# Performance work log

Measured on AMD Instinct MI355X. Metric: run time of the kernel, lower is better.

Reference implementation:

```python
import jax, jax.numpy as jnp
import numpy as np

D = 2048
H = 16
DH = D // H  # 128
B = 512
EPS = 1e-5


def _layernorm(x, g, b):
    m = jnp.mean(x, axis=-1, keepdims=True)
    v = jnp.mean((x - m) ** 2, axis=-1, keepdims=True)
    return (x - m) * jax.lax.rsqrt(v + EPS) * g + b


def setup_inputs() -> dict:
    key = jax.random.key(0)
    ks = jax.random.split(key, 16)
    s_in = 1.0 / np.sqrt(D)
    s_ff = 1.0 / np.sqrt(4 * D)
    return {
        "x": jax.random.normal(ks[0], (B, D), jnp.float32),
        # per-head q/k/v projections, stacked over heads: [H, D, DH]
        "Wq": jax.random.uniform(ks[1], (H, D, DH), jnp.float32, -s_in, s_in),
        "bq": jax.random.uniform(ks[2], (H, DH), jnp.float32, -s_in, s_in),
        "Wk": jax.random.uniform(ks[3], (H, D, DH), jnp.float32, -s_in, s_in),
        "bk": jax.random.uniform(ks[4], (H, DH), jnp.float32, -s_in, s_in),
        "Wv": jax.random.uniform(ks[5], (H, D, DH), jnp.float32, -s_in, s_in),
        "bv": jax.random.uniform(ks[6], (H, DH), jnp.float32, -s_in, s_in),
        "Wo": jax.random.uniform(ks[7], (D, D), jnp.float32, -s_in, s_in),
        "bo": jax.random.uniform(ks[8], (D,), jnp.float32, -s_in, s_in),
        "W1": jax.random.uniform(ks[9], (D, 4 * D), jnp.float32, -s_in, s_in),
        "b1": jax.random.uniform(ks[10], (4 * D,), jnp.float32, -s_in, s_in),
        "W2": jax.random.uniform(ks[11], (4 * D, D), jnp.float32, -s_ff, s_ff),
        "b2": jax.random.uniform(ks[12], (D,), jnp.float32, -s_ff, s_ff),
        "g1": jnp.ones((D,), jnp.float32),
        "be1": jnp.zeros((D,), jnp.float32),
        "g2": jnp.ones((D,), jnp.float32),
        "be2": jnp.zeros((D,), jnp.float32),
    }


def reference(x, Wq, bq, Wk, bk, Wv, bv, Wo, bo, W1, b1, W2, b2, g1, be1, g2, be2):
    # --- pre-norm attention branch ---
    h = _layernorm(x, g1, be1)                       # [B, D]
    q = jnp.einsum('bd,hde->bhe', h, Wq) + bq        # [B, H, DH]
    k = jnp.einsum('bd,hde->bhe', h, Wk) + bk
    v = jnp.einsum('bd,hde->bhe', h, Wv) + bv
    # outer-product 'attention' per sample: [B, H, DH, DH]
    attn = q[..., :, None] * k[..., None, :] / jnp.sqrt(jnp.float32(DH))
    attn = jax.nn.softmax(attn, axis=-1)
    o = jnp.einsum('bhij,bhj->bhi', attn, v)         # [B, H, DH]
    o = o.reshape(x.shape[0], H * DH)                # concat over heads
    x = x + o @ Wo + bo
    # --- pre-norm FFN branch ---
    h2 = _layernorm(x, g2, be2)
    x = x + jax.nn.relu(h2 @ W1 + b1) @ W2 + b2
    return x
```

## Files before the change

kernel.cpp:

```cpp
#include <hip/hip_runtime.h>
#include <hip/hip_bf16.h>
#include <math.h>


#define DDIM 2048
#define HHEADS 16
#define DHEAD 128
#define BROWS 512
#define LN_EPS 1e-5f

typedef __bf16 bf16x8_t __attribute__((ext_vector_type(8)));
typedef float f32x4_t __attribute__((ext_vector_type(4)));

#define GLD16(gptr, lptr)                                                     \
    __builtin_amdgcn_global_load_lds(                                         \
        (const __attribute__((address_space(1))) void*)(gptr),                \
        (__attribute__((address_space(3))) void*)(lptr), 16, 0, 0)

__global__ __launch_bounds__(256) void ln_kernel(const float* __restrict__ x,
                                                 const float* __restrict__ g,
                                                 const float* __restrict__ b,
                                                 __bf16* __restrict__ out) {
    const int row = blockIdx.x;
    const int tid = threadIdx.x;
    const float4* x4 = (const float4*)(x + (size_t)row * DDIM);
    float4 a = x4[2 * tid];
    float4 c = x4[2 * tid + 1];
    float s  = a.x + a.y + a.z + a.w + c.x + c.y + c.z + c.w;
    float s2 = a.x*a.x + a.y*a.y + a.z*a.z + a.w*a.w
             + c.x*c.x + c.y*c.y + c.z*c.z + c.w*c.w;
    #pragma unroll
    for (int off = 32; off > 0; off >>= 1) {
        s  += __shfl_down(s, off);
        s2 += __shfl_down(s2, off);
    }
    __shared__ float ps[4], ps2[4];
    __shared__ float mean_s, rstd_s;
    const int lane = tid & 63, w = tid >> 6;
    if (lane == 0) { ps[w] = s; ps2[w] = s2; }
    __syncthreads();
    if (tid == 0) {
        float S  = ps[0] + ps[1] + ps[2] + ps[3];
        float S2 = ps2[0] + ps2[1] + ps2[2] + ps2[3];
        float m  = S * (1.0f / DDIM);
        float var = S2 * (1.0f / DDIM) - m * m;
        mean_s = m;
        rstd_s = rsqrtf(var + LN_EPS);
    }
    __syncthreads();
    const float m = mean_s, r = rstd_s;
    const float4* g4 = (const float4*)g;
    const float4* b4 = (const float4*)b;
    float4 ga = g4[2 * tid], gb = g4[2 * tid + 1];
    float4 ba = b4[2 * tid], bb = b4[2 * tid + 1];
    bf16x8_t o;
    o[0] = (__bf16)((a.x - m) * r * ga.x + ba.x);
    o[1] = (__bf16)((a.y - m) * r * ga.y + ba.y);
    o[2] = (__bf16)((a.z - m) * r * ga.z + ba.z);
    o[3] = (__bf16)((a.w - m) * r * ga.w + ba.w);
    o[4] = (__bf16)((c.x - m) * r * gb.x + bb.x);
    o[5] = (__bf16)((c.y - m) * r * gb.y + bb.y);
    o[6] = (__bf16)((c.z - m) * r * gb.z + bb.z);
    o[7] = (__bf16)((c.w - m) * r * gb.w + bb.w);
    *(bf16x8_t*)(out + (size_t)row * DDIM + tid * 8) = o;
}

__global__ __launch_bounds__(256) void transpose_kernel(
    const float* __restrict__ src, __bf16* __restrict__ dst, int R, int C) {
    __shared__ float tile[32][33];
    const size_t bofs = (size_t)blockIdx.z * R * C;
    src += bofs;
    dst += bofs;
    const int c0 = blockIdx.x * 32, r0 = blockIdx.y * 32;
    const int tx = threadIdx.x & 31, ty = threadIdx.x >> 5;
    #pragma unroll
    for (int i = 0; i < 32; i += 8)
        tile[ty + i][tx] = src[(size_t)(r0 + ty + i) * C + c0 + tx];
    __syncthreads();
    #pragma unroll
    for (int i = 0; i < 32; i += 8)
        dst[(size_t)(c0 + ty + i) * R + r0 + tx] = (__bf16)tile[tx][ty + i];
}

__global__ __launch_bounds__(256) void fuse_bias_kernel(
    const float* __restrict__ bq, const float* __restrict__ bk,
    const float* __restrict__ bv, float* __restrict__ fb) {
    const int i = blockIdx.x * 256 + threadIdx.x;
    float v;
    if (i < 2048) v = bq[i];
    else if (i < 4096) v = bk[i - 2048];
    else v = bv[i - 4096];
    fb[i] = v;
}

template <int TM, int TN, int OUT_BF16, int RELU, int RES>
__global__ __launch_bounds__(256) void gemm_bt(
    const __bf16* __restrict__ A, int K,
    const __bf16* __restrict__ Bt,
    const float* __restrict__ bias,
    const float* __restrict__ Res,
    void* __restrict__ Cout, int N) {
    constexpr int DEPTH = 4;
    constexpr int STG = (TM + TN) * 32;
    __shared__ __align__(16) __bf16 smem[DEPTH * STG];

    const int tid = threadIdx.x;
    const int w = tid >> 6, lane = tid & 63;
    const int m0 = blockIdx.y * TM, n0 = blockIdx.x * TN;

    constexpr int NA = TM / 16;
    constexpr int NT = (TM + TN) / 16;
    constexpr int NI = NT / 4;

    const int sub_r = lane >> 2;
    const int sub_k = (lane & 3) * 8;

    const __bf16* srcs[NI];
    int toff[NI];
    #pragma unroll
    for (int i = 0; i < NI; i++) {
        const int t = w + 4 * i;
        toff[i] = t * 512;
        if (t < NA)
            srcs[i] = A + (size_t)(m0 + t * 16 + sub_r) * K + sub_k;
        else
            srcs[i] = Bt + (size_t)(n0 + (t - NA) * 16 + sub_r) * K + sub_k;
    }

    constexpr int MI = TM / 32;
    constexpr int NJ = TN / 32;
    const int wm = (w >> 1) * (TM / 2), wn = (w & 1) * (TN / 2);
    const int fm = lane & 15, quad = lane >> 4;

    f32x4_t acc[MI][NJ] = {};

    const int NK = K / 32;

    #pragma unroll
    for (int d = 0; d < DEPTH; d++)
        #pragma unroll
        for (int i = 0; i < NI; i++)
            GLD16(srcs[i] + d * 32, smem + d * STG + toff[i]);

    for (int ks = 0; ks < NK; ks++) {
        const __bf16* st = smem + (ks & (DEPTH - 1)) * STG;
        asm volatile("s_waitcnt vmcnt(%0)\n\ts_barrier"
                     :: "i"((DEPTH - 1) * NI) : "memory");

        bf16x8_t a[MI], b[NJ];
        #pragma unroll
        for (int i = 0; i < MI; i++)
            a[i] = *(const bf16x8_t*)&st[(wm + i * 16 + fm) * 32 + quad * 8];
        #pragma unroll
        for (int j = 0; j < NJ; j++)
            b[j] = *(const bf16x8_t*)&st[TM * 32 + (wn + j * 16 + fm) * 32 + quad * 8];
        #pragma unroll
        for (int i = 0; i < MI; i++)
            #pragma unroll
            for (int j = 0; j < NJ; j++)
                acc[i][j] = __builtin_amdgcn_mfma_f32_16x16x32_bf16(
                    a[i], b[j], acc[i][j], 0, 0, 0);

        asm volatile("s_waitcnt lgkmcnt(0)\n\ts_barrier" ::: "memory");
        if (ks + DEPTH < NK) {
            __bf16* dst = smem + (ks & (DEPTH - 1)) * STG;
            #pragma unroll
            for (int i = 0; i < NI; i++)
                GLD16(srcs[i] + (ks + DEPTH) * 32, dst + toff[i]);
        }
    }

    #pragma unroll
    for (int i = 0; i < MI; i++) {
        #pragma unroll
        for (int j = 0; j < NJ; j++) {
            const int col = n0 + wn + j * 16 + fm;
            const float bcol = bias[col];
            #pragma unroll
            for (int r = 0; r < 4; r++) {
                const int row = m0 + wm + i * 16 + quad * 4 + r;
                float val = acc[i][j][r] + bcol;
                if (RES) val += Res[(size_t)row * N + col];
                if (RELU) val = fmaxf(val, 0.0f);
                if (OUT_BF16)
                    ((__bf16*)Cout)[(size_t)row * N + col] = (__bf16)val;
                else
                    ((float*)Cout)[(size_t)row * N + col] = val;
            }
        }
    }
}

__global__ __launch_bounds__(128) void attn_kernel(
    const __bf16* __restrict__ qkv, __bf16* __restrict__ o) {
    const int bh = blockIdx.x;
    const int b = bh >> 4, h = bh & 15;
    const size_t base = (size_t)b * (3 * DDIM) + h * DHEAD;
    const int tid = threadIdx.x;
    __shared__ float ks[DHEAD], vs[DHEAD];
    ks[tid] = (float)qkv[base + DDIM + tid];
    vs[tid] = (float)qkv[base + 2 * DDIM + tid];
    __syncthreads();
    const float a = (float)qkv[base + tid] * 0.08838834764831845f;
    float den = 0.0f, num = 0.0f;
    #pragma unroll 8
    for (int j = 0; j < DHEAD; j++) {
        float e = __expf(a * ks[j]);
        den += e;
        num += e * vs[j];
    }
    o[(size_t)b * DDIM + h * DHEAD + tid] = (__bf16)(num / den);
}

extern "C" void kernel_launch(void* const* d_in, const int* in_sizes, int n_in,
                              void* d_out, int out_size, void* d_ws, size_t ws_size,
                              hipStream_t stream) {
    const float* x   = (const float*)d_in[0];
    const float* Wq  = (const float*)d_in[1];
    const float* bq  = (const float*)d_in[2];
    const float* Wk  = (const float*)d_in[3];
    const float* bk  = (const float*)d_in[4];
    const float* Wv  = (const float*)d_in[5];
    const float* bv  = (const float*)d_in[6];
    const float* Wo  = (const float*)d_in[7];
    const float* bo  = (const float*)d_in[8];
    const float* W1  = (const float*)d_in[9];
    const float* b1  = (const float*)d_in[10];
    const float* W2  = (const float*)d_in[11];
    const float* b2  = (const float*)d_in[12];
    const float* g1  = (const float*)d_in[13];
    const float* be1 = (const float*)d_in[14];
    const float* g2  = (const float*)d_in[15];
    const float* be2 = (const float*)d_in[16];
    float* out = (float*)d_out;

    char* base = (char*)d_ws;
    float*  fb     = (float*)(base + 0);
    __bf16* bt_qkv = (__bf16*)(base + 32768);
    char*   slotA  = base + 32768 + 25165824;
    char*   slotB  = slotA + 33554432;
    __bf16* h   = (__bf16*)(slotB + 0);
    __bf16* qkv = (__bf16*)(slotB + 2097152);
    __bf16* ob  = (__bf16*)(slotB + 8388608);
    float*  x1  = (float*)((char*)bt_qkv + 0);
    __bf16* h2  = (__bf16*)((char*)bt_qkv + 4194304);
    __bf16* t   = (__bf16*)((char*)bt_qkv + 6291456);
    __bf16* Wot = (__bf16*)slotA;
    __bf16* W1t = (__bf16*)slotB;
    __bf16* W2t = (__bf16*)slotA;

    fuse_bias_kernel<<<24, 256, 0, stream>>>(bq, bk, bv, fb);

    transpose_kernel<<<dim3(4, 64, 16), 256, 0, stream>>>(Wq, bt_qkv, DDIM, DHEAD);
    transpose_kernel<<<dim3(4, 64, 16), 256, 0, stream>>>(Wk, bt_qkv + 2048 * 2048, DDIM, DHEAD);
    transpose_kernel<<<dim3(4, 64, 16), 256, 0, stream>>>(Wv, bt_qkv + 2 * 2048 * 2048, DDIM, DHEAD);
    transpose_kernel<<<dim3(64, 64, 1), 256, 0, stream>>>(Wo, Wot, DDIM, DDIM);

    ln_kernel<<<BROWS, 256, 0, stream>>>(x, g1, be1, h);

    gemm_bt<64, 128, 1, 0, 0><<<dim3(48, 8), 256, 0, stream>>>(
        h, DDIM, bt_qkv, fb, nullptr, qkv, 3 * DDIM);

    attn_kernel<<<BROWS * HHEADS, 128, 0, stream>>>(qkv, ob);

    gemm_bt<64, 64, 0, 0, 1><<<dim3(32, 8), 256, 0, stream>>>(
        ob, DDIM, Wot, bo, x, x1, DDIM);

    transpose_kernel<<<dim3(256, 64, 1), 256, 0, stream>>>(W1, W1t, DDIM, 4 * DDIM);
    transpose_kernel<<<dim3(64, 256, 1), 256, 0, stream>>>(W2, W2t, 4 * DDIM, DDIM);

    ln_kernel<<<BROWS, 256, 0, stream>>>(x1, g2, be2, h2);

    gemm_bt<64, 128, 1, 1, 0><<<dim3(64, 8), 256, 0, stream>>>(
        h2, DDIM, W1t, b1, nullptr, t, 4 * DDIM);

    gemm_bt<64, 64, 0, 0, 1><<<dim3(32, 8), 256, 0, stream>>>(
        t, 4 * DDIM, W2t, b2, x1, out, DDIM);
}
```

Baseline: 401.0 us.

## Rework GEMM tiling with K=64 swizzled stages, split-K, and vectorized transpose

```diff
diff --git a/kernel.cpp b/kernel.cpp
--- a/kernel.cpp
+++ b/kernel.cpp
@@ -67,19 +67,33 @@
 
 __global__ __launch_bounds__(256) void transpose_kernel(
     const float* __restrict__ src, __bf16* __restrict__ dst, int R, int C) {
-    __shared__ float tile[32][33];
+    __shared__ float tile[64][65];
     const size_t bofs = (size_t)blockIdx.z * R * C;
     src += bofs;
     dst += bofs;
-    const int c0 = blockIdx.x * 32, r0 = blockIdx.y * 32;
-    const int tx = threadIdx.x & 31, ty = threadIdx.x >> 5;
-    #pragma unroll
-    for (int i = 0; i < 32; i += 8)
-        tile[ty + i][tx] = src[(size_t)(r0 + ty + i) * C + c0 + tx];
+    const int c0 = blockIdx.x * 64, r0 = blockIdx.y * 64;
+    const int t = threadIdx.x;
+    const int rr = t >> 4, cc = (t & 15) * 4;
+    #pragma unroll
+    for (int p = 0; p < 4; p++) {
+        const float4 v =
+            *(const float4*)(src + (size_t)(r0 + rr + 16 * p) * C + c0 + cc);
+        tile[rr + 16 * p][cc]     = v.x;
+        tile[rr + 16 * p][cc + 1] = v.y;
+        tile[rr + 16 * p][cc + 2] = v.z;
+        tile[rr + 16 * p][cc + 3] = v.w;
+    }
     __syncthreads();
-    #pragma unroll
-    for (int i = 0; i < 32; i += 8)
-        dst[(size_t)(c0 + ty + i) * R + r0 + tx] = (__bf16)tile[tx][ty + i];
+    const int slot = t & 7;
+    #pragma unroll
+    for (int p = 0; p < 2; p++) {
+        const int c = (t >> 3) + 32 * p;
+        bf16x8_t o;
+        #pragma unroll
+        for (int j = 0; j < 8; j++)
+            o[j] = (__bf16)tile[slot * 8 + j][c];
+        *(bf16x8_t*)(dst + (size_t)(c0 + c) * R + r0 + slot * 8) = o;
+    }
 }
 
 __global__ __launch_bounds__(256) void fuse_bias_kernel(
@@ -93,27 +107,29 @@
     fb[i] = v;
 }
 
-template <int TM, int TN, int OUT_BF16, int RELU, int RES>
+template <int TM, int TN, int DEPTH, int SPLITZ, int OUT_BF16, int RELU, int RES>
 __global__ __launch_bounds__(256) void gemm_bt(
     const __bf16* __restrict__ A, int K,
     const __bf16* __restrict__ Bt,
     const float* __restrict__ bias,
     const float* __restrict__ Res,
     void* __restrict__ Cout, int N) {
-    constexpr int DEPTH = 4;
-    constexpr int STG = (TM + TN) * 32;
+    constexpr int STG = (TM + TN) * 64;
     __shared__ __align__(16) __bf16 smem[DEPTH * STG];
 
     const int tid = threadIdx.x;
     const int w = tid >> 6, lane = tid & 63;
     const int m0 = blockIdx.y * TM, n0 = blockIdx.x * TN;
 
-    constexpr int NA = TM / 16;
-    constexpr int NT = (TM + TN) / 16;
+    const int Kloc = K / SPLITZ;
+    const int kb = blockIdx.z * Kloc;
+    const int NK = Kloc / 64;
+
+    constexpr int NT = (TM + TN) / 8;
     constexpr int NI = NT / 4;
 
-    const int sub_r = lane >> 2;
-    const int sub_k = (lane & 3) * 8;
+    const int srow = lane >> 3;
+    const int sslot = (lane & 7) ^ srow;
 
     const __bf16* srcs[NI];
     int toff[NI];
@@ -121,74 +137,121 @@
     for (int i = 0; i < NI; i++) {
         const int t = w + 4 * i;
         toff[i] = t * 512;
-        if (t < NA)
-            srcs[i] = A + (size_t)(m0 + t * 16 + sub_r) * K + sub_k;
-        else
-            srcs[i] = Bt + (size_t)(n0 + (t - NA) * 16 + sub_r) * K + sub_k;
+        const int r = t * 8 + srow;
+        srcs[i] = (r < TM)
+                      ? A + (size_t)(m0 + r) * K + kb + sslot * 8
+                      : Bt + (size_t)(n0 + r - TM) * K + kb + sslot * 8;
     }
 
     constexpr int MI = TM / 32;
     constexpr int NJ = TN / 32;
     const int wm = (w >> 1) * (TM / 2), wn = (w & 1) * (TN / 2);
     const int fm = lane & 15, quad = lane >> 4;
+    const int f7 = fm & 7;
+
+    int aoff[2][MI], boff[2][NJ];
+    #pragma unroll
+    for (int h = 0; h < 2; h++) {
+        const int sl = ((h * 4 + quad) ^ f7) * 16;
+        #pragma unroll
+        for (int i = 0; i < MI; i++)
+            aoff[h][i] = (wm + 16 * i + fm) * 128 + sl;
+        #pragma unroll
+        for (int j = 0; j < NJ; j++)
+            boff[h][j] = (TM + wn + 16 * j + fm) * 128 + sl;
+    }
 
     f32x4_t acc[MI][NJ] = {};
 
-    const int NK = K / 32;
-
     #pragma unroll
     for (int d = 0; d < DEPTH; d++)
         #pragma unroll
         for (int i = 0; i < NI; i++)
-            GLD16(srcs[i] + d * 32, smem + d * STG + toff[i]);
+            GLD16(srcs[i] + d * 64, smem + d * STG + toff[i]);
 
     for (int ks = 0; ks < NK; ks++) {
-        const __bf16* st = smem + (ks & (DEPTH - 1)) * STG;
+        const char* st = (const char*)smem + (ks % DEPTH) * (STG * 2);
         asm volatile("s_waitcnt vmcnt(%0)\n\ts_barrier"
                      :: "i"((DEPTH - 1) * NI) : "memory");
 
-        bf16x8_t a[MI], b[NJ];
+        bf16x8_t a[2][MI], b[2][NJ];
+        #pragma unroll
+        for (int h = 0; h < 2; h++) {
+            #pragma unroll
+            for (int i = 0; i < MI; i++)
+                a[h][i] = *(const bf16x8_t*)(st + aoff[h][i]);
+            #pragma unroll
+            for (int j = 0; j < NJ; j++)
+                b[h][j] = *(const bf16x8_t*)(st + boff[h][j]);
+        }
         #pragma unroll
         for (int i = 0; i < MI; i++)
-            a[i] = *(const bf16x8_t*)&st[(wm + i * 16 + fm) * 32 + quad * 8];
-        #pragma unroll
-        for (int j = 0; j < NJ; j++)
-            b[j] = *(const bf16x8_t*)&st[TM * 32 + (wn + j * 16 + fm) * 32 + quad * 8];
-        #pragma unroll
-        for (int i = 0; i < MI; i++)
-            #pragma unroll
-            for (int j = 0; j < NJ; j++)
+            #pragma unroll
+            for (int j = 0; j < NJ; j++) {
                 acc[i][j] = __builtin_amdgcn_mfma_f32_16x16x32_bf16(
-                    a[i], b[j], acc[i][j], 0, 0, 0);
+                    a[0][i], b[0][j], acc[i][j], 0, 0, 0);
+                acc[i][j] = __builtin_amdgcn_mfma_f32_16x16x32_bf16(
+                    a[1][i], b[1][j], acc[i][j], 0, 0, 0);
+            }
 
         asm volatile("s_waitcnt lgkmcnt(0)\n\ts_barrier" ::: "memory");
         if (ks + DEPTH < NK) {
-            __bf16* dst = smem + (ks & (DEPTH - 1)) * STG;
+            __bf16* dst = smem + (ks % DEPTH) * STG;
             #pragma unroll
             for (int i = 0; i < NI; i++)
-                GLD16(srcs[i] + (ks + DEPTH) * 32, dst + toff[i]);
+                GLD16(srcs[i] + (size_t)(ks + DEPTH) * 64, dst + toff[i]);
         }
     }
 
-    #pragma unroll
-    for (int i = 0; i < MI; i++) {
-        #pragma unroll
-        for (int j = 0; j < NJ; j++) {
-            const int col = n0 + wn + j * 16 + fm;
-            const float bcol = bias[col];
-            #pragma unroll
-            for (int r = 0; r < 4; r++) {
-                const int row = m0 + wm + i * 16 + quad * 4 + r;
-                float val = acc[i][j][r] + bcol;
-                if (RES) val += Res[(size_t)row * N + col];
-                if (RELU) val = fmaxf(val, 0.0f);
-                if (OUT_BF16)
-                    ((__bf16*)Cout)[(size_t)row * N + col] = (__bf16)val;
-                else
-                    ((float*)Cout)[(size_t)row * N + col] = val;
+    if (SPLITZ > 1) {
+        float* P = (float*)Cout + (size_t)blockIdx.z * (gridDim.y * TM) * N;
+        #pragma unroll
+        for (int i = 0; i < MI; i++)
+            #pragma unroll
+            for (int j = 0; j < NJ; j++) {
+                const int col = n0 + wn + 16 * j + fm;
+                #pragma unroll
+                for (int r = 0; r < 4; r++) {
+                    const int row = m0 + wm + 16 * i + quad * 4 + r;
+                    P[(size_t)row * N + col] = acc[i][j][r];
+                }
             }
-        }
-    }
+    } else {
+        #pragma unroll
+        for (int i = 0; i < MI; i++)
+            #pragma unroll
+            for (int j = 0; j < NJ; j++) {
+                const int col = n0 + wn + 16 * j + fm;
+                const float bcol = bias[col];
+                #pragma unroll
+                for (int r = 0; r < 4; r++) {
+                    const int row = m0 + wm + 16 * i + quad * 4 + r;
+                    float val = acc[i][j][r] + bcol;
+                    if (RES) val += Res[(size_t)row * N + col];
+                    if (RELU) val = fmaxf(val, 0.0f);
+                    if (OUT_BF16)
+                        ((__bf16*)Cout)[(size_t)row * N + col] = (__bf16)val;
+                    else
+                        ((float*)Cout)[(size_t)row * N + col] = val;
+                }
+            }
+    }
+}
+
+template <int NS>
+__global__ __launch_bounds__(256) void reduce_splitk(
+    const float* __restrict__ part, const float* __restrict__ Res,
+    const float* __restrict__ bias, float* __restrict__ out) {
+    const int idx = blockIdx.x * 256 + threadIdx.x;
+    const float4 b4 = ((const float4*)bias)[idx & 511];
+    float4 r = ((const float4*)Res)[idx];
+    #pragma unroll
+    for (int s = 0; s < NS; s++) {
+        const float4 p = ((const float4*)part)[(size_t)s * 262144 + idx];
+        r.x += p.x; r.y += p.y; r.z += p.z; r.w += p.w;
+    }
+    r.x += b4.x; r.y += b4.y; r.z += b4.z; r.w += b4.w;
+    ((float4*)out)[idx] = r;
 }
 
 __global__ __launch_bounds__(128) void attn_kernel(
@@ -242,6 +305,8 @@
     __bf16* h   = (__bf16*)(slotB + 0);
     __bf16* qkv = (__bf16*)(slotB + 2097152);
     __bf16* ob  = (__bf16*)(slotB + 8388608);
+    float*  woP = (float*)(slotB + 10485760);
+    float*  w2P = (float*)(slotB + 0);
     float*  x1  = (float*)((char*)bt_qkv + 0);
     __bf16* h2  = (__bf16*)((char*)bt_qkv + 4194304);
     __bf16* t   = (__bf16*)((char*)bt_qkv + 6291456);
@@ -251,29 +316,31 @@
 
     fuse_bias_kernel<<<24, 256, 0, stream>>>(bq, bk, bv, fb);
 
-    transpose_kernel<<<dim3(4, 64, 16), 256, 0, stream>>>(Wq, bt_qkv, DDIM, DHEAD);
-    transpose_kernel<<<dim3(4, 64, 16), 256, 0, stream>>>(Wk, bt_qkv + 2048 * 2048, DDIM, DHEAD);
-    transpose_kernel<<<dim3(4, 64, 16), 256, 0, stream>>>(Wv, bt_qkv + 2 * 2048 * 2048, DDIM, DHEAD);
-    transpose_kernel<<<dim3(64, 64, 1), 256, 0, stream>>>(Wo, Wot, DDIM, DDIM);
+    transpose_kernel<<<dim3(2, 32, 16), 256, 0, stream>>>(Wq, bt_qkv, DDIM, DHEAD);
+    transpose_kernel<<<dim3(2, 32, 16), 256, 0, stream>>>(Wk, bt_qkv + 2048 * 2048, DDIM, DHEAD);
+    transpose_kernel<<<dim3(2, 32, 16), 256, 0, stream>>>(Wv, bt_qkv + 2 * 2048 * 2048, DDIM, DHEAD);
+    transpose_kernel<<<dim3(32, 32, 1), 256, 0, stream>>>(Wo, Wot, DDIM, DDIM);
 
     ln_kernel<<<BROWS, 256, 0, stream>>>(x, g1, be1, h);
 
-    gemm_bt<64, 128, 1, 0, 0><<<dim3(48, 8), 256, 0, stream>>>(
+    gemm_bt<128, 128, 3, 1, 1, 0, 0><<<dim3(48, 4), 256, 0, stream>>>(
         h, DDIM, bt_qkv, fb, nullptr, qkv, 3 * DDIM);
 
     attn_kernel<<<BROWS * HHEADS, 128, 0, stream>>>(qkv, ob);
 
-    gemm_bt<64, 64, 0, 0, 1><<<dim3(32, 8), 256, 0, stream>>>(
-        ob, DDIM, Wot, bo, x, x1, DDIM);
-
-    transpose_kernel<<<dim3(256, 64, 1), 256, 0, stream>>>(W1, W1t, DDIM, 4 * DDIM);
-    transpose_kernel<<<dim3(64, 256, 1), 256, 0, stream>>>(W2, W2t, 4 * DDIM, DDIM);
+    gemm_bt<64, 128, 4, 2, 0, 0, 0><<<dim3(16, 8, 2), 256, 0, stream>>>(
+        ob, DDIM, Wot, nullptr, nullptr, woP, DDIM);
+    reduce_splitk<2><<<1024, 256, 0, stream>>>(woP, x, bo, x1);
+
+    transpose_kernel<<<dim3(128, 32, 1), 256, 0, stream>>>(W1, W1t, DDIM, 4 * DDIM);
+    transpose_kernel<<<dim3(32, 128, 1), 256, 0, stream>>>(W2, W2t, 4 * DDIM, DDIM);
 
     ln_kernel<<<BROWS, 256, 0, stream>>>(x1, g2, be2, h2);
 
-    gemm_bt<64, 128, 1, 1, 0><<<dim3(64, 8), 256, 0, stream>>>(
+    gemm_bt<128, 128, 3, 1, 1, 1, 0><<<dim3(64, 4), 256, 0, stream>>>(
         h2, DDIM, W1t, b1, nullptr, t, 4 * DDIM);
 
-    gemm_bt<64, 64, 0, 0, 1><<<dim3(32, 8), 256, 0, stream>>>(
-        t, 4 * DDIM, W2t, b2, x1, out, DDIM);
-}
+    gemm_bt<128, 128, 3, 4, 0, 0, 0><<<dim3(16, 4, 4), 256, 0, stream>>>(
+        t, 4 * DDIM, W2t, nullptr, nullptr, w2P, DDIM);
+    reduce_splitk<4><<<1024, 256, 0, stream>>>(w2P, x1, b2, out);
+}
```

Result: faster. 367.4 us (-8.4%).
